# Performance work log

Hardware: AMD Instinct MI355X
Metric: run time of the kernel (lower is better)

Reference implementation:

```python
import jax, jax.numpy as jnp
import numpy as np

T, B, D, H, NQ = 512, 256, 256, 256, 4  # note H == B is required by the original torch broadcasting


def setup_inputs() -> dict:
    key = jax.random.key(0)
    ks = jax.random.split(key, 9)
    inp = {"inputs": jax.random.normal(ks[0], (T, B, D), jnp.float32)}
    names = ["forget", "input", "update", "output"]
    for j, n in enumerate(names):
        inp[f"W_{n}"] = jax.random.normal(ks[1 + j], (NQ, D + H), jnp.float32) * 0.05
        inp[f"b_{n}"] = jnp.zeros((NQ,), jnp.float32)
        inp[f"phi_{n}"] = jax.random.uniform(ks[5 + j], (NQ,), jnp.float32, 0.0, 2.0 * np.pi)
    return inp


def _qgate(z, phi):
    # 4-qubit circuit on |0000>: RX(z_j) then trainable RX(phi_j) on each wire
    # (two RX on the same wire compose: angle theta_j = z_j + phi_j), then the
    # CNOT ring (0->1,1->2,2->3,3->0), then <Z_0>.
    # Heisenberg picture: conjugating Z_0 back through the CNOT ring gives
    # Z_0 -> Z_1 Z_2 Z_3, and on the product state <Z_j> = cos(theta_j), so
    # <Z_0> = cos(theta_1) * cos(theta_2) * cos(theta_3)  (wire 0 drops out).
    c = jnp.cos(z + phi)  # [B, 4]
    return c[:, 1] * c[:, 2] * c[:, 3]  # [B]


def reference(inputs, W_forget, b_forget, phi_forget, W_input, b_input, phi_input,
              W_update, b_update, phi_update, W_output, b_output, phi_output):
    bsz = inputs.shape[1]
    hx = jnp.zeros((bsz, H), inputs.dtype)
    cx = jnp.zeros((bsz, H), inputs.dtype)

    def step(carry, x):
        hx, cx = carry
        comb = jnp.concatenate([x, hx], axis=1)  # [B, D+H]
        f = jax.nn.sigmoid(_qgate(comb @ W_forget.T + b_forget, phi_forget))   # [B]
        i = jax.nn.sigmoid(_qgate(comb @ W_input.T + b_input, phi_input))      # [B]
        g = jnp.tanh(_qgate(comb @ W_update.T + b_update, phi_update))         # [B]
        o = jax.nn.sigmoid(_qgate(comb @ W_output.T + b_output, phi_output))   # [B]
        # [B] * [B,H] broadcasts the gate over the hidden axis (valid since H == B,
        # exactly matching the original torch semantics)
        cx = f * cx + i * g
        hx = o * jnp.tanh(cx)
        return (hx, cx), hx

    (hx, cx), outs = jax.lax.scan(step, (hx, cx), inputs)
    return outs, hx, cx
```

## Files before the change

### kernel.cpp

```cpp
#include <hip/hip_runtime.h>


#define T_DIM 512
#define B_DIM 256
#define D_DIM 256
#define H_DIM 256
#define DH    512
#define NG    16
#define PAD   260

__device__ __forceinline__ float fast_sigmoid(float x) {
    return 1.0f / (1.0f + __expf(-x));
}
__device__ __forceinline__ float fast_tanh(float x) {
    float e = __expf(2.0f * x);
    return (e - 1.0f) / (e + 1.0f);
}
template <int CTRL, int RM, int BM, bool BC>
__device__ __forceinline__ float dadd(float x) {
    return x + __int_as_float(
        __builtin_amdgcn_update_dpp(0, __float_as_int(x), CTRL, RM, BM, BC));
}
__device__ __forceinline__ float wsum(float x) {
    x = dadd<0x111, 0xf, 0xf, true >(x);
    x = dadd<0x112, 0xf, 0xf, true >(x);
    x = dadd<0x114, 0xf, 0xf, true >(x);
    x = dadd<0x118, 0xf, 0xf, true >(x);
    x = dadd<0x142, 0xa, 0xf, false>(x);
    x = dadd<0x143, 0xc, 0xf, false>(x);
    return x;
}
__device__ __forceinline__ void lds_barrier() {
    __asm__ volatile("s_waitcnt lgkmcnt(0)\n\ts_barrier" ::: "memory");
}

__global__ __launch_bounds__(256) void zx_kernel(
    const float* __restrict__ x,
    const float* __restrict__ Wf, const float* __restrict__ Wi,
    const float* __restrict__ Wu, const float* __restrict__ Wo,
    const float* __restrict__ bf, const float* __restrict__ bi,
    const float* __restrict__ bu, const float* __restrict__ bo,
    const float* __restrict__ phf, const float* __restrict__ phi,
    const float* __restrict__ phu, const float* __restrict__ pho,
    float* __restrict__ zx)
{
    __shared__ float Wl[NG][PAD];
    __shared__ float Xl[16][PAD];
    const int tid = threadIdx.x;

    for (int e = tid; e < NG * 64; e += 256) {
        int q16 = e >> 6, c4 = (e & 63) * 4;
        int g = q16 >> 2, qj = q16 & 3;
        const float* W = (g == 0) ? Wf : (g == 1) ? Wi : (g == 2) ? Wu : Wo;
        *(float4*)&Wl[q16][c4] = *(const float4*)(W + qj * DH + c4);
    }
    const long base = (long)blockIdx.x * 16 * D_DIM;
    for (int e = tid; e < 16 * 64; e += 256) {
        int r = e >> 6, c4 = (e & 63) * 4;
        *(float4*)&Xl[r][c4] = *(const float4*)(x + base + r * D_DIM + c4);
    }
    __syncthreads();

    const int q16 = tid & 15, r = tid >> 4;
    const int g = q16 >> 2, qj = q16 & 3;
    const float* bv = (g == 0) ? bf : (g == 1) ? bi : (g == 2) ? bu : bo;
    const float* pv = (g == 0) ? phf : (g == 1) ? phi : (g == 2) ? phu : pho;
    float acc = bv[qj] + pv[qj];
    #pragma unroll 4
    for (int k = 0; k < D_DIM; k += 4) {
        float4 xv = *(float4*)&Xl[r][k];
        float4 wv = *(float4*)&Wl[q16][k];
        acc += xv.x * wv.x + xv.y * wv.y + xv.z * wv.z + xv.w * wv.w;
    }
    zx[(long)blockIdx.x * 256 + tid] = acc;
}

__global__ __launch_bounds__(512) void rec_kernel(
    const float* __restrict__ Wf, const float* __restrict__ Wi,
    const float* __restrict__ Wu, const float* __restrict__ Wo,
    const float* __restrict__ zx,
    float* __restrict__ hv_tab,
    float* __restrict__ c_fin)
{
    __shared__ float Hbuf[2][H_DIM];
    __shared__ __align__(16) float zh_s[2][8];
    const int tid  = threadIdx.x;
    const int lane = tid & 63;
    const int wv   = tid >> 6;
    const int h    = tid >> 1;
    const int half = tid & 1;
    const int l4   = lane * 4;

    float4 WA = make_float4(0,0,0,0), WB = WA;
    if (wv < 6) {
        const int cA = 2 * wv, cB = cA + 1;
        const int gA = cA / 3, jA = cA % 3 + 1;
        const int gB = cB / 3, jB = cB % 3 + 1;
        const float* WgA = (gA == 0) ? Wf : (gA == 1) ? Wi : (gA == 2) ? Wu : Wo;
        const float* WgB = (gB == 0) ? Wf : (gB == 1) ? Wi : (gB == 2) ? Wu : Wo;
        WA = *(const float4*)(WgA + jA * DH + 256 + l4);
        WB = *(const float4*)(WgB + jB * DH + 256 + l4);
    }

    float C = 0.0f, Hprev = 0.0f;
    if (tid < H_DIM) Hbuf[1][tid] = 0.0f;
    __syncthreads();

    float4 za0, za1, zb0, zb1;
    {
        const float4* p0 = (const float4*)(zx + (long)h * NG) + half * 2;
        const float4* p1 = (const float4*)(zx + ((long)B_DIM + h) * NG) + half * 2;
        za0 = p0[0]; za1 = p0[1];
        zb0 = p1[0]; zb1 = p1[1];
    }

    auto step = [&](int t, float4& z0, float4& z1) {
        if (half) hv_tab[(long)(t - 1) * H_DIM + h] = Hprev;

        if (wv < 6) {
            const float4 Hv4 = *(const float4*)&Hbuf[(t + 1) & 1][l4];
            float pA = fmaf(WA.x, Hv4.x, fmaf(WA.y, Hv4.y, fmaf(WA.z, Hv4.z, WA.w * Hv4.w)));
            float pB = fmaf(WB.x, Hv4.x, fmaf(WB.y, Hv4.y, fmaf(WB.z, Hv4.z, WB.w * Hv4.w)));
            pA = wsum(pA);
            pB = wsum(pB);
            if (lane == 63) {
                const int cA = 2 * wv;
                zh_s[cA / 6][cA % 6]       = pA;
                zh_s[(cA + 1) / 6][(cA + 1) % 6] = pB;
            }
        }
        lds_barrier();

        const float4 ZA = *(const float4*)&zh_s[half][0];
        const float2 ZB = *(const float2*)&zh_s[half][4];
        const float c1 = __cosf(z0.y + ZA.x), c2 = __cosf(z0.z + ZA.y), c3 = __cosf(z0.w + ZA.z);
        const float c4 = __cosf(z1.y + ZA.w), c5 = __cosf(z1.z + ZB.x), c6 = __cosf(z1.w + ZB.y);
        const float pA = c1 * c2 * c3, pB = c4 * c5 * c6;
        float gA, gB;
        if (half == 0) { gA = fast_sigmoid(pA); gB = fast_sigmoid(pB); }
        else           { gA = fast_tanh(pA);    gB = fast_sigmoid(pB); }
        const float oA = __shfl_xor(gA, 1);
        const float oB = __shfl_xor(gB, 1);
        const float f_ = half ? oA : gA;
        const float i_ = half ? oB : gB;
        const float g_ = half ? gA : oA;
        const float o_ = half ? gB : oB;

        {
            const int tp = (t + 2 < T_DIM) ? (t + 2) : t;
            const float4* pp = (const float4*)(zx + ((long)tp * B_DIM + h) * NG) + half * 2;
            z0 = pp[0]; z1 = pp[1];
        }

        C = fmaf(f_, C, i_ * g_);
        const float Hnew = o_ * fast_tanh(C);
        if (half == 0) Hbuf[t & 1][h] = Hnew;
        Hprev = Hnew;
        lds_barrier();
    };

    for (int t = 0; t < T_DIM; t += 2) {
        step(t,     za0, za1);
        step(t + 1, zb0, zb1);
    }

    if (half) {
        hv_tab[(long)(T_DIM - 1) * H_DIM + h] = Hprev;
        c_fin[h] = C;
    }
}

__global__ __launch_bounds__(256) void bc_kernel(
    const float* __restrict__ hv_tab, const float* __restrict__ c_fin,
    float* __restrict__ out)
{
    const int blk  = blockIdx.x;
    const int w    = threadIdx.x >> 6;
    const int lane = threadIdx.x & 63;

    const float* src;
    long base;
    int rbase;
    if (blk < 4 * T_DIM) {
        const int t = blk >> 2;
        rbase = (blk & 3) * 64;
        src = hv_tab + (long)t * H_DIM;
        base = (long)t * (B_DIM * H_DIM);
    } else {
        const int k = blk - 4 * T_DIM;
        rbase = (k & 3) * 64;
        src = (k < 4) ? (hv_tab + (long)(T_DIM - 1) * H_DIM) : c_fin;
        base = (long)T_DIM * (B_DIM * H_DIM) + (k < 4 ? 0 : (long)B_DIM * H_DIM);
    }
    const float4 v = ((const float4*)src)[lane];
    #pragma unroll
    for (int it = 0; it < 16; ++it) {
        const int row = rbase + w + 4 * it;
        ((float4*)(out + base + (long)row * H_DIM))[lane] = v;
    }
}

extern "C" void kernel_launch(void* const* d_in, const int* in_sizes, int n_in,
                              void* d_out, int out_size, void* d_ws, size_t ws_size,
                              hipStream_t stream) {
    (void)in_sizes; (void)n_in; (void)out_size; (void)ws_size;
    const float* x   = (const float*)d_in[0];
    const float* Wf  = (const float*)d_in[1];
    const float* bf  = (const float*)d_in[2];
    const float* phf = (const float*)d_in[3];
    const float* Wi  = (const float*)d_in[4];
    const float* bi  = (const float*)d_in[5];
    const float* phi = (const float*)d_in[6];
    const float* Wu  = (const float*)d_in[7];
    const float* bu  = (const float*)d_in[8];
    const float* phu = (const float*)d_in[9];
    const float* Wo  = (const float*)d_in[10];
    const float* bo  = (const float*)d_in[11];
    const float* pho = (const float*)d_in[12];

    float* zx     = (float*)d_ws;
    float* hv_pad = zx + (size_t)T_DIM * B_DIM * NG;
    float* hv_tab = hv_pad + H_DIM;
    float* c_fin  = hv_tab + (size_t)T_DIM * H_DIM;

    zx_kernel<<<(T_DIM * B_DIM) / 16, 256, 0, stream>>>(
        x, Wf, Wi, Wu, Wo, bf, bi, bu, bo, phf, phi, phu, pho, zx);

    rec_kernel<<<1, 512, 0, stream>>>(
        Wf, Wi, Wu, Wo, zx, hv_tab, c_fin);

    bc_kernel<<<4 * T_DIM + 8, 256, 0, stream>>>(hv_tab, c_fin, (float*)d_out);
}
```

Baseline: 631.7 us.

## Fuse recurrent matvec into gate step with LDS atomics, one barrier per step

Each thread now owns one hidden unit and keeps its six recurrent weights in registers. After computing the new hidden value it does a 32-lane DPP reduction per weight and atomically adds the partial sums into a triple-buffered LDS accumulator. This removes the Hbuf exchange and one of the two barriers per timestep, shortening the serial critical path. The cost is LDS atomic contention from 16 half-waves per step and a zero-reset of the next buffer, which relies on the triple-buffer rotation being correct.

```diff
diff --git a/kernel.cpp b/kernel.cpp
--- a/kernel.cpp
+++ b/kernel.cpp
@@ -21,13 +21,12 @@
     return x + __int_as_float(
         __builtin_amdgcn_update_dpp(0, __float_as_int(x), CTRL, RM, BM, BC));
 }
-__device__ __forceinline__ float wsum(float x) {
+__device__ __forceinline__ float rsum32(float x) {
     x = dadd<0x111, 0xf, 0xf, true >(x);
     x = dadd<0x112, 0xf, 0xf, true >(x);
     x = dadd<0x114, 0xf, 0xf, true >(x);
     x = dadd<0x118, 0xf, 0xf, true >(x);
     x = dadd<0x142, 0xa, 0xf, false>(x);
-    x = dadd<0x143, 0xc, 0xf, false>(x);
     return x;
 }
 __device__ __forceinline__ void lds_barrier() {
@@ -82,29 +81,26 @@
     float* __restrict__ hv_tab,
     float* __restrict__ c_fin)
 {
-    __shared__ float Hbuf[2][H_DIM];
-    __shared__ __align__(16) float zh_s[2][8];
+    __shared__ float zh_s[3][2][8];
     const int tid  = threadIdx.x;
     const int lane = tid & 63;
     const int wv   = tid >> 6;
-    const int h    = tid >> 1;
-    const int half = tid & 1;
-    const int l4   = lane * 4;
-
-    float4 WA = make_float4(0,0,0,0), WB = WA;
-    if (wv < 6) {
-        const int cA = 2 * wv, cB = cA + 1;
-        const int gA = cA / 3, jA = cA % 3 + 1;
-        const int gB = cB / 3, jB = cB % 3 + 1;
-        const float* WgA = (gA == 0) ? Wf : (gA == 1) ? Wi : (gA == 2) ? Wu : Wo;
-        const float* WgB = (gB == 0) ? Wf : (gB == 1) ? Wi : (gB == 2) ? Wu : Wo;
-        WA = *(const float4*)(WgA + jA * DH + 256 + l4);
-        WB = *(const float4*)(WgB + jB * DH + 256 + l4);
-    }
+    const int l31  = lane & 31;
+    const int half = lane >> 5;
+    const int h    = wv * 32 + l31;
+
+    float W6[6];
+    #pragma unroll
+    for (int k = 0; k < 6; ++k) {
+        const int c = half * 6 + k;
+        const int g = c / 3, j = c % 3 + 1;
+        const float* Wg = (g == 0) ? Wf : (g == 1) ? Wi : (g == 2) ? Wu : Wo;
+        W6[k] = Wg[j * DH + 256 + h];
+    }
+
+    if (tid < 48) ((float*)zh_s)[tid] = 0.0f;
 
     float C = 0.0f, Hprev = 0.0f;
-    if (tid < H_DIM) Hbuf[1][tid] = 0.0f;
-    __syncthreads();
 
     float4 za0, za1, zb0, zb1;
     {
@@ -113,34 +109,27 @@
         za0 = p0[0]; za1 = p0[1];
         zb0 = p1[0]; zb1 = p1[1];
     }
+    lds_barrier();
 
     auto step = [&](int t, float4& z0, float4& z1) {
+        const int rb = t % 3;
+        const int wb = (t + 1) % 3;
+        const int zb = (t + 2) % 3;
+
+        const float4 ZA = *(const float4*)&zh_s[rb][half][0];
+        const float2 ZB = *(const float2*)&zh_s[rb][half][4];
+
         if (half) hv_tab[(long)(t - 1) * H_DIM + h] = Hprev;
-
-        if (wv < 6) {
-            const float4 Hv4 = *(const float4*)&Hbuf[(t + 1) & 1][l4];
-            float pA = fmaf(WA.x, Hv4.x, fmaf(WA.y, Hv4.y, fmaf(WA.z, Hv4.z, WA.w * Hv4.w)));
-            float pB = fmaf(WB.x, Hv4.x, fmaf(WB.y, Hv4.y, fmaf(WB.z, Hv4.z, WB.w * Hv4.w)));
-            pA = wsum(pA);
-            pB = wsum(pB);
-            if (lane == 63) {
-                const int cA = 2 * wv;
-                zh_s[cA / 6][cA % 6]       = pA;
-                zh_s[(cA + 1) / 6][(cA + 1) % 6] = pB;
-            }
-        }
-        lds_barrier();
-
-        const float4 ZA = *(const float4*)&zh_s[half][0];
-        const float2 ZB = *(const float2*)&zh_s[half][4];
+        if (wv == 0 && lane < 16) zh_s[zb][lane >> 3][lane & 7] = 0.0f;
+
         const float c1 = __cosf(z0.y + ZA.x), c2 = __cosf(z0.z + ZA.y), c3 = __cosf(z0.w + ZA.z);
         const float c4 = __cosf(z1.y + ZA.w), c5 = __cosf(z1.z + ZB.x), c6 = __cosf(z1.w + ZB.y);
         const float pA = c1 * c2 * c3, pB = c4 * c5 * c6;
         float gA, gB;
         if (half == 0) { gA = fast_sigmoid(pA); gB = fast_sigmoid(pB); }
         else           { gA = fast_tanh(pA);    gB = fast_sigmoid(pB); }
-        const float oA = __shfl_xor(gA, 1);
-        const float oB = __shfl_xor(gB, 1);
+        const float oA = __shfl_xor(gA, 32);
+        const float oB = __shfl_xor(gB, 32);
         const float f_ = half ? oA : gA;
         const float i_ = half ? oB : gB;
         const float g_ = half ? gA : oA;
@@ -154,8 +143,20 @@
 
         C = fmaf(f_, C, i_ * g_);
         const float Hnew = o_ * fast_tanh(C);
-        if (half == 0) Hbuf[t & 1][h] = Hnew;
         Hprev = Hnew;
+
+        const float p0 = rsum32(W6[0] * Hnew);
+        const float p1 = rsum32(W6[1] * Hnew);
+        const float p2 = rsum32(W6[2] * Hnew);
+        const float p3 = rsum32(W6[3] * Hnew);
+        const float p4 = rsum32(W6[4] * Hnew);
+        const float p5 = rsum32(W6[5] * Hnew);
+        if (l31 == 31) {
+            float* dst = &zh_s[wb][half][0];
+            atomicAdd(dst + 0, p0); atomicAdd(dst + 1, p1);
+            atomicAdd(dst + 2, p2); atomicAdd(dst + 3, p3);
+            atomicAdd(dst + 4, p4); atomicAdd(dst + 5, p5);
+        }
         lds_barrier();
     };
 
```

Result: no change. 643.2 us (+1.8%).

## Register-block zx projection over 256 rows per block and use DPP for lane swap

Applied to the files above, without the earlier changes.

The input projection kernel now has each block handle 256 rows, staging K in chunks of 64 through shared memory. Each thread computes a 4x4 register tile, so every loaded weight and input vector is reused four times, and results go out as float4 stores. Separately, the pairwise gate exchange in the recurrent kernel swaps __shfl_xor for a DPP quad-permute, which cuts latency on the serial critical path. The larger tile uses about 74 KB of LDS per block and launches only 512 blocks, which may reduce occupancy.

```diff
diff --git a/kernel.cpp b/kernel.cpp
--- a/kernel.cpp
+++ b/kernel.cpp
@@ -7,7 +7,7 @@
 #define H_DIM 256
 #define DH    512
 #define NG    16
-#define PAD   260
+#define XPAD  68
 
 __device__ __forceinline__ float fast_sigmoid(float x) {
     return 1.0f / (1.0f + __expf(-x));
@@ -29,6 +29,10 @@
     x = dadd<0x142, 0xa, 0xf, false>(x);
     x = dadd<0x143, 0xc, 0xf, false>(x);
     return x;
+}
+__device__ __forceinline__ float dpp_xor1(float x) {
+    return __int_as_float(
+        __builtin_amdgcn_update_dpp(0, __float_as_int(x), 0xB1, 0xf, 0xf, true));
 }
 __device__ __forceinline__ void lds_barrier() {
     __asm__ volatile("s_waitcnt lgkmcnt(0)\n\ts_barrier" ::: "memory");
@@ -44,35 +48,69 @@
     const float* __restrict__ phu, const float* __restrict__ pho,
     float* __restrict__ zx)
 {
-    __shared__ float Wl[NG][PAD];
-    __shared__ float Xl[16][PAD];
+    __shared__ float Xc[256][XPAD];
+    __shared__ float Wc[NG][XPAD];
     const int tid = threadIdx.x;
-
-    for (int e = tid; e < NG * 64; e += 256) {
-        int q16 = e >> 6, c4 = (e & 63) * 4;
-        int g = q16 >> 2, qj = q16 & 3;
-        const float* W = (g == 0) ? Wf : (g == 1) ? Wi : (g == 2) ? Wu : Wo;
-        *(float4*)&Wl[q16][c4] = *(const float4*)(W + qj * DH + c4);
-    }
-    const long base = (long)blockIdx.x * 16 * D_DIM;
-    for (int e = tid; e < 16 * 64; e += 256) {
-        int r = e >> 6, c4 = (e & 63) * 4;
-        *(float4*)&Xl[r][c4] = *(const float4*)(x + base + r * D_DIM + c4);
-    }
-    __syncthreads();
-
-    const int q16 = tid & 15, r = tid >> 4;
-    const int g = q16 >> 2, qj = q16 & 3;
-    const float* bv = (g == 0) ? bf : (g == 1) ? bi : (g == 2) ? bu : bo;
-    const float* pv = (g == 0) ? phf : (g == 1) ? phi : (g == 2) ? phu : pho;
-    float acc = bv[qj] + pv[qj];
-    #pragma unroll 4
-    for (int k = 0; k < D_DIM; k += 4) {
-        float4 xv = *(float4*)&Xl[r][k];
-        float4 wv = *(float4*)&Wl[q16][k];
-        acc += xv.x * wv.x + xv.y * wv.y + xv.z * wv.z + xv.w * wv.w;
-    }
-    zx[(long)blockIdx.x * 256 + tid] = acc;
+    const int rt  = tid >> 2;
+    const int qt  = tid & 3;
+
+    const float* bv = (qt == 0) ? bf : (qt == 1) ? bi : (qt == 2) ? bu : bo;
+    const float* pv = (qt == 0) ? phf : (qt == 1) ? phi : (qt == 2) ? phu : pho;
+    float acc[4][4];
+    #pragma unroll
+    for (int j = 0; j < 4; ++j) {
+        const float bj = bv[j] + pv[j];
+        acc[0][j] = bj; acc[1][j] = bj; acc[2][j] = bj; acc[3][j] = bj;
+    }
+
+    const long base = (long)blockIdx.x * 256 * D_DIM;
+
+    for (int c = 0; c < 4; ++c) {
+        const int k0 = c * 64;
+        #pragma unroll
+        for (int it = 0; it < 16; ++it) {
+            const int e = tid + it * 256;
+            const int row = e >> 4, col4 = (e & 15) * 4;
+            *(float4*)&Xc[row][col4] =
+                *(const float4*)(x + base + (long)row * D_DIM + k0 + col4);
+        }
+        {
+            const int q16 = tid >> 4, col4 = (tid & 15) * 4;
+            const int g = q16 >> 2, qj = q16 & 3;
+            const float* W = (g == 0) ? Wf : (g == 1) ? Wi : (g == 2) ? Wu : Wo;
+            *(float4*)&Wc[q16][col4] = *(const float4*)(W + qj * DH + k0 + col4);
+        }
+        __syncthreads();
+
+        #pragma unroll 4
+        for (int kk = 0; kk < 16; ++kk) {
+            const int k4 = kk * 4;
+            float4 xv0 = *(float4*)&Xc[rt][k4];
+            float4 xv1 = *(float4*)&Xc[rt +  64][k4];
+            float4 xv2 = *(float4*)&Xc[rt + 128][k4];
+            float4 xv3 = *(float4*)&Xc[rt + 192][k4];
+            float4 wv0 = *(float4*)&Wc[4 * qt + 0][k4];
+            float4 wv1 = *(float4*)&Wc[4 * qt + 1][k4];
+            float4 wv2 = *(float4*)&Wc[4 * qt + 2][k4];
+            float4 wv3 = *(float4*)&Wc[4 * qt + 3][k4];
+            #pragma unroll
+            for (int i = 0; i < 4; ++i) {
+                const float4 xv = (i == 0) ? xv0 : (i == 1) ? xv1 : (i == 2) ? xv2 : xv3;
+                acc[i][0] = fmaf(xv.x, wv0.x, fmaf(xv.y, wv0.y, fmaf(xv.z, wv0.z, fmaf(xv.w, wv0.w, acc[i][0]))));
+                acc[i][1] = fmaf(xv.x, wv1.x, fmaf(xv.y, wv1.y, fmaf(xv.z, wv1.z, fmaf(xv.w, wv1.w, acc[i][1]))));
+                acc[i][2] = fmaf(xv.x, wv2.x, fmaf(xv.y, wv2.y, fmaf(xv.z, wv2.z, fmaf(xv.w, wv2.w, acc[i][2]))));
+                acc[i][3] = fmaf(xv.x, wv3.x, fmaf(xv.y, wv3.y, fmaf(xv.z, wv3.z, fmaf(xv.w, wv3.w, acc[i][3]))));
+            }
+        }
+        __syncthreads();
+    }
+
+    const long orow = (long)blockIdx.x * 256;
+    #pragma unroll
+    for (int i = 0; i < 4; ++i) {
+        *(float4*)&zx[(orow + rt + 64 * i) * NG + qt * 4] =
+            make_float4(acc[i][0], acc[i][1], acc[i][2], acc[i][3]);
+    }
 }
 
 __global__ __launch_bounds__(512) void rec_kernel(
@@ -125,7 +163,7 @@
             pB = wsum(pB);
             if (lane == 63) {
                 const int cA = 2 * wv;
-                zh_s[cA / 6][cA % 6]       = pA;
+                zh_s[cA / 6][cA % 6]             = pA;
                 zh_s[(cA + 1) / 6][(cA + 1) % 6] = pB;
             }
         }
@@ -139,8 +177,8 @@
         float gA, gB;
         if (half == 0) { gA = fast_sigmoid(pA); gB = fast_sigmoid(pB); }
         else           { gA = fast_tanh(pA);    gB = fast_sigmoid(pB); }
-        const float oA = __shfl_xor(gA, 1);
-        const float oB = __shfl_xor(gB, 1);
+        const float oA = dpp_xor1(gA);
+        const float oB = dpp_xor1(gB);
         const float f_ = half ? oA : gA;
         const float i_ = half ? oB : gB;
         const float g_ = half ? gA : oA;
@@ -223,7 +261,7 @@
     float* hv_tab = hv_pad + H_DIM;
     float* c_fin  = hv_tab + (size_t)T_DIM * H_DIM;
 
-    zx_kernel<<<(T_DIM * B_DIM) / 16, 256, 0, stream>>>(
+    zx_kernel<<<T_DIM, 256, 0, stream>>>(
         x, Wf, Wi, Wu, Wo, bf, bi, bu, bo, phf, phi, phu, pho, zx);
 
     rec_kernel<<<1, 512, 0, stream>>>(
```

After: 599.7 us. -5.1%, faster.
